# Performance work log

Hardware: AMD Instinct MI355X
Metric: run time of the kernel (lower is better)

## Reference

```python
import jax, jax.numpy as jnp
import numpy as np

N_NODES = 50000
N_EDGES = 800000
D_FEAT = 96


def setup_inputs() -> dict:
    key = jax.random.key(0)
    k1, k2, k3, k4 = jax.random.split(key, 4)
    features = jax.random.normal(k1, (N_NODES, D_FEAT), dtype=jnp.float32)
    edge_rows = jax.random.randint(k2, (N_EDGES,), 0, N_NODES, dtype=jnp.int64)
    edge_cols = jax.random.randint(k3, (N_EDGES,), 0, N_NODES, dtype=jnp.int64)
    edge_vals = jnp.ones((N_EDGES,), dtype=jnp.float32)
    # torch semantics (new_features[index] = out_features) require len(index) == N,
    # i.e. index is a permutation of arange(N) in real usage.
    index = jax.random.permutation(k4, N_NODES).astype(jnp.int64)
    return {"features": features, "edge_rows": edge_rows, "edge_cols": edge_cols,
            "edge_vals": edge_vals, "index": index}


def reference(features, edge_rows, edge_cols, edge_vals, index):
    N = features.shape[0]
    # normalize_adj: D^{-1/2} A D^{-1/2}, rowsum-based, inf -> 0
    deg = jax.ops.segment_sum(edge_vals, edge_rows, num_segments=N)  # [N]
    safe_deg = jnp.where(deg > 0, deg, 1.0)
    d_inv_sqrt = jnp.where(deg > 0, jax.lax.rsqrt(safe_deg), 0.0)
    norm_vals = edge_vals * d_inv_sqrt[edge_rows] * d_inv_sqrt[edge_cols]  # [E]
    # spmm(A_norm, features): gather source rows, scale, scatter-add to dest rows
    msgs = features[edge_cols] * norm_vals[:, None]                 # [E, D]
    out_features = jax.ops.segment_sum(msgs, edge_rows, num_segments=N)  # [N, D]
    # new_features[index] = out_features; rows not covered by index keep old features
    present = jnp.zeros((N,), dtype=bool).at[index].set(True)
    scattered = jnp.zeros_like(features).at[index].set(out_features)
    new_features = jnp.where(present[:, None], scattered, features)
    return new_features
```

## Files before the change

### kernel.cpp

```cpp
#include <hip/hip_runtime.h>
#include <hip/hip_fp16.h>

#define N_NODES 50000
#define N_EDGES 800000
#define D_FEAT  96
#define NBUCK   196
#define NCHB    256
#define CHUNK   (N_EDGES / NCHB)
#define KMAX    6144
#define N4      (N_NODES * D_FEAT / 4)

typedef float    f32x4 __attribute__((ext_vector_type(4)));
typedef unsigned u32x2 __attribute__((ext_vector_type(2)));

__device__ __forceinline__ int block_excl_scan_256(int v, int tid, int* ws4) {
    int lane = tid & 63, wid = tid >> 6;
    int x = v;
    for (int off = 1; off < 64; off <<= 1) {
        int t = __shfl_up(x, off);
        if (lane >= off) x += t;
    }
    if (lane == 63) ws4[wid] = x;
    __syncthreads();
    int add = 0;
    for (int w = 0; w < wid; ++w) add += ws4[w];
    __syncthreads();
    return x + add - v;
}

__device__ __forceinline__ float2 up2(unsigned u) {
    __half2 h = *reinterpret_cast<__half2*>(&u);
    return __half22float2(h);
}

__device__ __forceinline__ void acc8(uint4 u, float w, float* a) {
    float2 f;
    f = up2(u.x); a[0] += f.x * w; a[1] += f.y * w;
    f = up2(u.y); a[2] += f.x * w; a[3] += f.y * w;
    f = up2(u.z); a[4] += f.x * w; a[5] += f.y * w;
    f = up2(u.w); a[6] += f.x * w; a[7] += f.y * w;
}

__global__ __launch_bounds__(256) void convert_hist_kernel(const float* __restrict__ feat,
                                                           uint2* __restrict__ ft,
                                                           const int* __restrict__ rows,
                                                           int* __restrict__ blockHist) {
    __shared__ int hist[NBUCK];
    int tid = threadIdx.x, b = blockIdx.x;
    for (int i = b * 256 + tid; i < N4; i += 1024 * 256) {
        f32x4 f = __builtin_nontemporal_load((const f32x4*)feat + i);
        __half2 h01 = __floats2half2_rn(f.x, f.y);
        __half2 h23 = __floats2half2_rn(f.z, f.w);
        ft[i] = make_uint2(*(unsigned*)&h01, *(unsigned*)&h23);
    }
    if (b < NCHB) {
        for (int t = tid; t < NBUCK; t += 256) hist[t] = 0;
        __syncthreads();
        int s = b * CHUNK;
        for (int k = tid; k < CHUNK; k += 256) atomicAdd(&hist[rows[s + k] >> 8], 1);
        __syncthreads();
        for (int t = tid; t < NBUCK; t += 256) blockHist[b * NBUCK + t] = hist[t];
    }
}

__global__ __launch_bounds__(256) void col_scan_kernel(int* __restrict__ blockHist,
                                                       int* __restrict__ btot) {
    __shared__ int ws4[4];
    int bin = blockIdx.x, j = threadIdx.x;
    int v = blockHist[j * NBUCK + bin];
    int ex = block_excl_scan_256(v, j, ws4);
    blockHist[j * NBUCK + bin] = ex;
    if (j == 255) btot[bin] = ex + v;
}

__global__ __launch_bounds__(256) void bucket_scan_kernel(const int* __restrict__ btot,
                                                          int* __restrict__ bbase,
                                                          int* __restrict__ offsets) {
    __shared__ int ws4[4];
    int t = threadIdx.x;
    int v = (t < NBUCK) ? btot[t] : 0;
    int ex = block_excl_scan_256(v, t, ws4);
    if (t < NBUCK) bbase[t] = ex;
    if (t == 0) { bbase[NBUCK] = N_EDGES; offsets[N_NODES] = N_EDGES; }
}

__global__ __launch_bounds__(256) void bucket_scatter_kernel(const int* __restrict__ rows,
                                                             const int* __restrict__ cols,
                                                             const float* __restrict__ vals,
                                                             const int* __restrict__ bbase,
                                                             const int* __restrict__ blockHist,
                                                             uint2* __restrict__ bb) {
    __shared__ int cur[NBUCK];
    int b = blockIdx.x, tid = threadIdx.x;
    for (int t = tid; t < NBUCK; t += 256)
        cur[t] = bbase[t] + blockHist[b * NBUCK + t];
    __syncthreads();
    int s = b * CHUNK;
    for (int k = tid; k < CHUNK; k += 256) {
        int e = s + k;
        int r = rows[e];
        unsigned c = (unsigned)cols[e];
        float v = vals[e];
        int pos = atomicAdd(&cur[r >> 8], 1);
        bb[pos] = make_uint2(((unsigned)(r & 255) << 16) | c, __float_as_uint(v));
    }
}

__global__ __launch_bounds__(256) void bucket_csr_kernel(const int* __restrict__ bbase,
                                                         uint2* __restrict__ bb,
                                                         int* __restrict__ offsets,
                                                         float* __restrict__ dis) {
    __shared__ uint2 stage[KMAX];
    __shared__ int   hist[256];
    __shared__ float degF[256];
    __shared__ int   ws4[4];
    int bin = blockIdx.x, tid = threadIdx.x;
    int start = bbase[bin], end = bbase[bin + 1];
    int cnt = min(end - start, KMAX);
    hist[tid] = 0;
    degF[tid] = 0.0f;
    __syncthreads();
    for (int k = tid; k < cnt; k += 256) {
        uint2 p = bb[start + k];
        stage[k] = p;
        int rl = p.x >> 16;
        atomicAdd(&hist[rl], 1);
        atomicAdd(&degF[rl], __uint_as_float(p.y));
    }
    __syncthreads();
    int v = hist[tid];
    int ex = block_excl_scan_256(v, tid, ws4);
    int row = bin * 256 + tid;
    if (row < N_NODES) {
        offsets[row] = start + ex;
        float d = degF[tid];
        dis[row] = (d > 0.0f) ? rsqrtf(d) : 0.0f;
    }
    __syncthreads();
    hist[tid] = ex;
    __syncthreads();
    for (int k = tid; k < cnt; k += 256) {
        uint2 p = stage[k];
        int rl = p.x >> 16;
        int pos = atomicAdd(&hist[rl], 1);
        bb[start + pos] = p;
    }
}

__global__ __launch_bounds__(256) void spmm_kernel(const uint4* __restrict__ ftab,
                                                   const int* __restrict__ offsets,
                                                   const uint2* __restrict__ pairs,
                                                   const float* __restrict__ dis,
                                                   const int* __restrict__ index,
                                                   float* __restrict__ out) {
    int gid  = blockIdx.x * 256 + threadIdx.x;
    int r    = gid / 12;
    int lane = gid % 12;
    if (r >= N_NODES) return;
    int s = offsets[r], t = offsets[r + 1];
    float a[8] = {0.f, 0.f, 0.f, 0.f, 0.f, 0.f, 0.f, 0.f};
    int e = s;
    for (; e + 3 < t; e += 4) {
        uint2 p0 = pairs[e], p1 = pairs[e + 1], p2 = pairs[e + 2], p3 = pairs[e + 3];
        unsigned c0 = p0.x & 0xFFFFu, c1 = p1.x & 0xFFFFu;
        unsigned c2 = p2.x & 0xFFFFu, c3 = p3.x & 0xFFFFu;
        float w0 = __uint_as_float(p0.y) * dis[c0];
        float w1 = __uint_as_float(p1.y) * dis[c1];
        float w2 = __uint_as_float(p2.y) * dis[c2];
        float w3 = __uint_as_float(p3.y) * dis[c3];
        uint4 u0 = ftab[c0 * 12u + lane];
        uint4 u1 = ftab[c1 * 12u + lane];
        uint4 u2 = ftab[c2 * 12u + lane];
        uint4 u3 = ftab[c3 * 12u + lane];
        acc8(u0, w0, a); acc8(u1, w1, a); acc8(u2, w2, a); acc8(u3, w3, a);
    }
    for (; e < t; ++e) {
        uint2 p0 = pairs[e];
        unsigned c0 = p0.x & 0xFFFFu;
        float w0 = __uint_as_float(p0.y) * dis[c0];
        uint4 u0 = ftab[c0 * 12u + lane];
        acc8(u0, w0, a);
    }
    float dr  = dis[r];
    int  orow = index[r];
    f32x4* op = (f32x4*)(out + (size_t)orow * D_FEAT) + lane * 2;
    f32x4 v0 = {a[0] * dr, a[1] * dr, a[2] * dr, a[3] * dr};
    f32x4 v1 = {a[4] * dr, a[5] * dr, a[6] * dr, a[7] * dr};
    __builtin_nontemporal_store(v0, op);
    __builtin_nontemporal_store(v1, op + 1);
}

extern "C" void kernel_launch(void* const* d_in, const int* in_sizes, int n_in,
                              void* d_out, int out_size, void* d_ws, size_t ws_size,
                              hipStream_t stream) {
    const float* features  = (const float*)d_in[0];
    const int*   edge_rows = (const int*)d_in[1];
    const int*   edge_cols = (const int*)d_in[2];
    const float* edge_vals = (const float*)d_in[3];
    const int*   index     = (const int*)d_in[4];
    float* out = (float*)d_out;

    unsigned* wsu     = (unsigned*)d_ws;
    uint2*    ft      = (uint2*)wsu;
    uint2*    bb      = (uint2*)(wsu + 2400000);
    int*      bhist   = (int*)(wsu + 4000000);
    int*      btot    = (int*)(wsu + 4050176);
    int*      bbase   = (int*)(wsu + 4050372);
    int*      offsets = (int*)(wsu + 4050569);
    float*    dis     = (float*)(wsu + 4100570);

    convert_hist_kernel<<<1024, 256, 0, stream>>>(features, ft, edge_rows, bhist);
    col_scan_kernel<<<NBUCK, 256, 0, stream>>>(bhist, btot);
    bucket_scan_kernel<<<1, 256, 0, stream>>>(btot, bbase, offsets);
    bucket_scatter_kernel<<<NCHB, 256, 0, stream>>>(edge_rows, edge_cols, edge_vals,
                                                    bbase, bhist, bb);
    bucket_csr_kernel<<<NBUCK, 256, 0, stream>>>(bbase, bb, offsets, dis);

    int total = N_NODES * 12;
    spmm_kernel<<<(total + 255) / 256, 256, 0, stream>>>((const uint4*)ft, offsets, bb,
                                                         dis, index, out);
}
```

Measured before the change: 71.97 us.

## Split fp32-to-fp16 conversion across scan kernels to fill idle blocks

The feature conversion no longer runs inside the histogram kernel. It is split into two halves that run as extra blocks in the column-scan and bucket-scan launches. Those small, latency-bound scan kernels use few blocks, so the bandwidth-bound conversion fills otherwise idle CUs, and the histogram kernel now launches only its needed blocks. In exchange the scan blocks may be delayed by conversion traffic, and launch sizes grow.

Result: slower. 75.43 us (+4.8%).

```diff
diff --git a/kernel.cpp b/kernel.cpp
--- a/kernel.cpp
+++ b/kernel.cpp
@@ -9,9 +9,12 @@
 #define CHUNK   (N_EDGES / NCHB)
 #define KMAX    6144
 #define N4      (N_NODES * D_FEAT / 4)
-
-typedef float    f32x4 __attribute__((ext_vector_type(4)));
-typedef unsigned u32x2 __attribute__((ext_vector_type(2)));
+#define CVT_PER_BLK 2048
+#define CBLK    ((N4 + CVT_PER_BLK - 1) / CVT_PER_BLK)
+#define CBLK1   (CBLK / 2)
+#define CBLK2   (CBLK - CBLK1)
+
+typedef float f32x4 __attribute__((ext_vector_type(4)));
 
 __device__ __forceinline__ int block_excl_scan_256(int v, int tid, int* ws4) {
     int lane = tid & 63, wid = tid >> 6;
@@ -41,30 +44,42 @@
     f = up2(u.w); a[6] += f.x * w; a[7] += f.y * w;
 }
 
-__global__ __launch_bounds__(256) void convert_hist_kernel(const float* __restrict__ feat,
-                                                           uint2* __restrict__ ft,
-                                                           const int* __restrict__ rows,
-                                                           int* __restrict__ blockHist) {
+__device__ __forceinline__ void convert_slice(const float* __restrict__ feat,
+                                              uint2* __restrict__ ft,
+                                              int cb, int tid) {
+    int base = cb * CVT_PER_BLK + tid;
+    #pragma unroll
+    for (int it = 0; it < CVT_PER_BLK / 256; ++it) {
+        int i = base + it * 256;
+        if (i < N4) {
+            f32x4 f = __builtin_nontemporal_load((const f32x4*)feat + i);
+            __half2 h01 = __floats2half2_rn(f.x, f.y);
+            __half2 h23 = __floats2half2_rn(f.z, f.w);
+            ft[i] = make_uint2(*(unsigned*)&h01, *(unsigned*)&h23);
+        }
+    }
+}
+
+__global__ __launch_bounds__(256) void hist_kernel(const int* __restrict__ rows,
+                                                   int* __restrict__ blockHist) {
     __shared__ int hist[NBUCK];
     int tid = threadIdx.x, b = blockIdx.x;
-    for (int i = b * 256 + tid; i < N4; i += 1024 * 256) {
-        f32x4 f = __builtin_nontemporal_load((const f32x4*)feat + i);
-        __half2 h01 = __floats2half2_rn(f.x, f.y);
-        __half2 h23 = __floats2half2_rn(f.z, f.w);
-        ft[i] = make_uint2(*(unsigned*)&h01, *(unsigned*)&h23);
-    }
-    if (b < NCHB) {
-        for (int t = tid; t < NBUCK; t += 256) hist[t] = 0;
-        __syncthreads();
-        int s = b * CHUNK;
-        for (int k = tid; k < CHUNK; k += 256) atomicAdd(&hist[rows[s + k] >> 8], 1);
-        __syncthreads();
-        for (int t = tid; t < NBUCK; t += 256) blockHist[b * NBUCK + t] = hist[t];
-    }
-}
-
-__global__ __launch_bounds__(256) void col_scan_kernel(int* __restrict__ blockHist,
-                                                       int* __restrict__ btot) {
+    for (int t = tid; t < NBUCK; t += 256) hist[t] = 0;
+    __syncthreads();
+    int s = b * CHUNK;
+    for (int k = tid; k < CHUNK; k += 256) atomicAdd(&hist[rows[s + k] >> 8], 1);
+    __syncthreads();
+    for (int t = tid; t < NBUCK; t += 256) blockHist[b * NBUCK + t] = hist[t];
+}
+
+__global__ __launch_bounds__(256) void col_scan_conv_kernel(int* __restrict__ blockHist,
+                                                            int* __restrict__ btot,
+                                                            const float* __restrict__ feat,
+                                                            uint2* __restrict__ ft) {
+    if (blockIdx.x >= NBUCK) {
+        convert_slice(feat, ft, blockIdx.x - NBUCK, threadIdx.x);
+        return;
+    }
     __shared__ int ws4[4];
     int bin = blockIdx.x, j = threadIdx.x;
     int v = blockHist[j * NBUCK + bin];
@@ -73,9 +88,15 @@
     if (j == 255) btot[bin] = ex + v;
 }
 
-__global__ __launch_bounds__(256) void bucket_scan_kernel(const int* __restrict__ btot,
-                                                          int* __restrict__ bbase,
-                                                          int* __restrict__ offsets) {
+__global__ __launch_bounds__(256) void bucket_scan_conv_kernel(const int* __restrict__ btot,
+                                                               int* __restrict__ bbase,
+                                                               int* __restrict__ offsets,
+                                                               const float* __restrict__ feat,
+                                                               uint2* __restrict__ ft) {
+    if (blockIdx.x > 0) {
+        convert_slice(feat, ft, CBLK1 + blockIdx.x - 1, threadIdx.x);
+        return;
+    }
     __shared__ int ws4[4];
     int t = threadIdx.x;
     int v = (t < NBUCK) ? btot[t] : 0;
@@ -209,9 +230,10 @@
     int*      offsets = (int*)(wsu + 4050569);
     float*    dis     = (float*)(wsu + 4100570);
 
-    convert_hist_kernel<<<1024, 256, 0, stream>>>(features, ft, edge_rows, bhist);
-    col_scan_kernel<<<NBUCK, 256, 0, stream>>>(bhist, btot);
-    bucket_scan_kernel<<<1, 256, 0, stream>>>(btot, bbase, offsets);
+    hist_kernel<<<NCHB, 256, 0, stream>>>(edge_rows, bhist);
+    col_scan_conv_kernel<<<NBUCK + CBLK1, 256, 0, stream>>>(bhist, btot, features, ft);
+    bucket_scan_conv_kernel<<<1 + CBLK2, 256, 0, stream>>>(btot, bbase, offsets,
+                                                           features, ft);
     bucket_scatter_kernel<<<NCHB, 256, 0, stream>>>(edge_rows, edge_cols, edge_vals,
                                                     bbase, bhist, bb);
     bucket_csr_kernel<<<NBUCK, 256, 0, stream>>>(bbase, bb, offsets, dis);
```

## Slice fp16 feature table into 8 column slabs and run sliced SpMM

Applied to the files above, without the earlier changes.

The fp16 feature table is re-laid out as 8 slices of 12 columns, each slice a contiguous [N,8-word] table padded to 32 bytes per row, so each slice is about 1.6 MB and may stay cache-resident. SpMM now assigns one thread per row per slice, with blocks interleaving slices, instead of 12 threads per row covering all 96 columns. The aim is better gather locality per slice. In exchange, the edge list, offsets and dis lookups are re-read 8 times, the 4-way unrolled edge loop is gone, per-thread work is serial over edges with uneven row lengths, and the table grows by a third because of padding.

Result: slower. 174.1 us (+142.0%).

```diff
diff --git a/kernel.cpp b/kernel.cpp
--- a/kernel.cpp
+++ b/kernel.cpp
@@ -8,10 +8,11 @@
 #define NCHB    256
 #define CHUNK   (N_EDGES / NCHB)
 #define KMAX    6144
-#define N4      (N_NODES * D_FEAT / 4)
-
-typedef float    f32x4 __attribute__((ext_vector_type(4)));
-typedef unsigned u32x2 __attribute__((ext_vector_type(2)));
+#define NSLICE  8
+#define SDIM    12
+#define NCONV   (N_NODES * NSLICE)
+
+typedef float f32x4 __attribute__((ext_vector_type(4)));
 
 __device__ __forceinline__ int block_excl_scan_256(int v, int tid, int* ws4) {
     int lane = tid & 63, wid = tid >> 6;
@@ -33,31 +34,38 @@
     return __half22float2(h);
 }
 
-__device__ __forceinline__ void acc8(uint4 u, float w, float* a) {
-    float2 f;
-    f = up2(u.x); a[0] += f.x * w; a[1] += f.y * w;
-    f = up2(u.y); a[2] += f.x * w; a[3] += f.y * w;
-    f = up2(u.z); a[4] += f.x * w; a[5] += f.y * w;
-    f = up2(u.w); a[6] += f.x * w; a[7] += f.y * w;
+__device__ __forceinline__ unsigned pk2(float x, float y) {
+    __half2 h = __floats2half2_rn(x, y);
+    return *reinterpret_cast<unsigned*>(&h);
 }
 
 __global__ __launch_bounds__(256) void convert_hist_kernel(const float* __restrict__ feat,
-                                                           uint2* __restrict__ ft,
+                                                           unsigned* __restrict__ ft8,
                                                            const int* __restrict__ rows,
                                                            int* __restrict__ blockHist) {
     __shared__ int hist[NBUCK];
     int tid = threadIdx.x, b = blockIdx.x;
-    for (int i = b * 256 + tid; i < N4; i += 1024 * 256) {
-        f32x4 f = __builtin_nontemporal_load((const f32x4*)feat + i);
-        __half2 h01 = __floats2half2_rn(f.x, f.y);
-        __half2 h23 = __floats2half2_rn(f.z, f.w);
-        ft[i] = make_uint2(*(unsigned*)&h01, *(unsigned*)&h23);
-    }
-    if (b < NCHB) {
+    bool doHist = (b < NCHB);
+    if (doHist) {
         for (int t = tid; t < NBUCK; t += 256) hist[t] = 0;
         __syncthreads();
-        int s = b * CHUNK;
-        for (int k = tid; k < CHUNK; k += 256) atomicAdd(&hist[rows[s + k] >> 8], 1);
+    }
+    int i = b * 256 + tid;
+    if (i < NCONV) {
+        int n = i >> 3, s = i & 7;
+        const f32x4* src = (const f32x4*)(feat + (size_t)n * D_FEAT + s * SDIM);
+        f32x4 fA = __builtin_nontemporal_load(src);
+        f32x4 fB = __builtin_nontemporal_load(src + 1);
+        f32x4 fC = __builtin_nontemporal_load(src + 2);
+        unsigned* dst = ft8 + (size_t)(s * N_NODES + n) * 8;
+        uint4 lo = make_uint4(pk2(fA.x, fA.y), pk2(fA.z, fA.w),
+                              pk2(fB.x, fB.y), pk2(fB.z, fB.w));
+        *(uint4*)dst = lo;
+        *(uint2*)(dst + 4) = make_uint2(pk2(fC.x, fC.y), pk2(fC.z, fC.w));
+    }
+    if (doHist) {
+        int sBase = b * CHUNK;
+        for (int k = tid; k < CHUNK; k += 256) atomicAdd(&hist[rows[sBase + k] >> 8], 1);
         __syncthreads();
         for (int t = tid; t < NBUCK; t += 256) blockHist[b * NBUCK + t] = hist[t];
     }
@@ -147,47 +155,43 @@
     }
 }
 
-__global__ __launch_bounds__(256) void spmm_kernel(const uint4* __restrict__ ftab,
-                                                   const int* __restrict__ offsets,
-                                                   const uint2* __restrict__ pairs,
-                                                   const float* __restrict__ dis,
-                                                   const int* __restrict__ index,
-                                                   float* __restrict__ out) {
-    int gid  = blockIdx.x * 256 + threadIdx.x;
-    int r    = gid / 12;
-    int lane = gid % 12;
+__global__ __launch_bounds__(256) void spmm_sliced_kernel(const unsigned* __restrict__ ft8,
+                                                          const int* __restrict__ offsets,
+                                                          const uint2* __restrict__ pairs,
+                                                          const float* __restrict__ dis,
+                                                          const int* __restrict__ index,
+                                                          float* __restrict__ out) {
+    int slice = blockIdx.x & 7;
+    int chunk = blockIdx.x >> 3;
+    int r = chunk * 256 + threadIdx.x;
     if (r >= N_NODES) return;
     int s = offsets[r], t = offsets[r + 1];
-    float a[8] = {0.f, 0.f, 0.f, 0.f, 0.f, 0.f, 0.f, 0.f};
-    int e = s;
-    for (; e + 3 < t; e += 4) {
-        uint2 p0 = pairs[e], p1 = pairs[e + 1], p2 = pairs[e + 2], p3 = pairs[e + 3];
-        unsigned c0 = p0.x & 0xFFFFu, c1 = p1.x & 0xFFFFu;
-        unsigned c2 = p2.x & 0xFFFFu, c3 = p3.x & 0xFFFFu;
-        float w0 = __uint_as_float(p0.y) * dis[c0];
-        float w1 = __uint_as_float(p1.y) * dis[c1];
-        float w2 = __uint_as_float(p2.y) * dis[c2];
-        float w3 = __uint_as_float(p3.y) * dis[c3];
-        uint4 u0 = ftab[c0 * 12u + lane];
-        uint4 u1 = ftab[c1 * 12u + lane];
-        uint4 u2 = ftab[c2 * 12u + lane];
-        uint4 u3 = ftab[c3 * 12u + lane];
-        acc8(u0, w0, a); acc8(u1, w1, a); acc8(u2, w2, a); acc8(u3, w3, a);
-    }
-    for (; e < t; ++e) {
-        uint2 p0 = pairs[e];
-        unsigned c0 = p0.x & 0xFFFFu;
-        float w0 = __uint_as_float(p0.y) * dis[c0];
-        uint4 u0 = ftab[c0 * 12u + lane];
-        acc8(u0, w0, a);
+    const unsigned* tab = ft8 + (size_t)slice * N_NODES * 8;
+    float a[SDIM] = {0.f, 0.f, 0.f, 0.f, 0.f, 0.f, 0.f, 0.f, 0.f, 0.f, 0.f, 0.f};
+    for (int e = s; e < t; ++e) {
+        uint2 p = pairs[e];
+        unsigned c = p.x & 0xFFFFu;
+        float w = __uint_as_float(p.y) * dis[c];
+        const unsigned* rec = tab + c * 8u;
+        uint4 u4 = *(const uint4*)rec;
+        uint2 u2 = *(const uint2*)(rec + 4);
+        float2 f;
+        f = up2(u4.x); a[0]  += f.x * w; a[1]  += f.y * w;
+        f = up2(u4.y); a[2]  += f.x * w; a[3]  += f.y * w;
+        f = up2(u4.z); a[4]  += f.x * w; a[5]  += f.y * w;
+        f = up2(u4.w); a[6]  += f.x * w; a[7]  += f.y * w;
+        f = up2(u2.x); a[8]  += f.x * w; a[9]  += f.y * w;
+        f = up2(u2.y); a[10] += f.x * w; a[11] += f.y * w;
     }
     float dr  = dis[r];
     int  orow = index[r];
-    f32x4* op = (f32x4*)(out + (size_t)orow * D_FEAT) + lane * 2;
-    f32x4 v0 = {a[0] * dr, a[1] * dr, a[2] * dr, a[3] * dr};
-    f32x4 v1 = {a[4] * dr, a[5] * dr, a[6] * dr, a[7] * dr};
+    f32x4* op = (f32x4*)(out + (size_t)orow * D_FEAT + slice * SDIM);
+    f32x4 v0 = {a[0] * dr, a[1] * dr, a[2]  * dr, a[3]  * dr};
+    f32x4 v1 = {a[4] * dr, a[5] * dr, a[6]  * dr, a[7]  * dr};
+    f32x4 v2 = {a[8] * dr, a[9] * dr, a[10] * dr, a[11] * dr};
     __builtin_nontemporal_store(v0, op);
     __builtin_nontemporal_store(v1, op + 1);
+    __builtin_nontemporal_store(v2, op + 2);
 }
 
 extern "C" void kernel_launch(void* const* d_in, const int* in_sizes, int n_in,
@@ -201,22 +205,22 @@
     float* out = (float*)d_out;
 
     unsigned* wsu     = (unsigned*)d_ws;
-    uint2*    ft      = (uint2*)wsu;
-    uint2*    bb      = (uint2*)(wsu + 2400000);
-    int*      bhist   = (int*)(wsu + 4000000);
-    int*      btot    = (int*)(wsu + 4050176);
-    int*      bbase   = (int*)(wsu + 4050372);
-    int*      offsets = (int*)(wsu + 4050569);
-    float*    dis     = (float*)(wsu + 4100570);
-
-    convert_hist_kernel<<<1024, 256, 0, stream>>>(features, ft, edge_rows, bhist);
+    unsigned* ft8     = wsu;
+    uint2*    bb      = (uint2*)(wsu + 3200000);
+    int*      bhist   = (int*)(wsu + 4800000);
+    int*      btot    = (int*)(wsu + 4850176);
+    int*      bbase   = (int*)(wsu + 4850372);
+    int*      offsets = (int*)(wsu + 4850569);
+    float*    dis     = (float*)(wsu + 4900570);
+
+    int cblk = (NCONV + 255) / 256;
+    convert_hist_kernel<<<cblk, 256, 0, stream>>>(features, ft8, edge_rows, bhist);
     col_scan_kernel<<<NBUCK, 256, 0, stream>>>(bhist, btot);
     bucket_scan_kernel<<<1, 256, 0, stream>>>(btot, bbase, offsets);
     bucket_scatter_kernel<<<NCHB, 256, 0, stream>>>(edge_rows, edge_cols, edge_vals,
                                                     bbase, bhist, bb);
     bucket_csr_kernel<<<NBUCK, 256, 0, stream>>>(bbase, bb, offsets, dis);
 
-    int total = N_NODES * 12;
-    spmm_kernel<<<(total + 255) / 256, 256, 0, stream>>>((const uint4*)ft, offsets, bb,
-                                                         dis, index, out);
-}
+    spmm_sliced_kernel<<<NSLICE * NBUCK, 256, 0, stream>>>(ft8, offsets, bb,
+                                                           dis, index, out);
+}
```
